# Performance work log

Measured on AMD Instinct MI355X. Metric: run time of the kernel, lower is better.

The kernel has to match this reference:

```python
import jax, jax.numpy as jnp
import numpy as np

V, H, B, T = 64, 128, 128, 512


def setup_inputs() -> dict:
    key = jax.random.key(0)
    ks = jax.random.split(key, 12)
    s = 0.05
    return {
        "x": jax.random.randint(ks[0], (B, T), 0, V),
        "emb": jax.random.normal(ks[1], (V, H), dtype=jnp.float32) * s,
        "w_ih_f": jax.random.normal(ks[2], (4 * H, H), dtype=jnp.float32) * s,
        "w_hh_f": jax.random.normal(ks[3], (4 * H, H), dtype=jnp.float32) * s,
        "b_ih_f": jax.random.normal(ks[4], (4 * H,), dtype=jnp.float32) * s,
        "b_hh_f": jax.random.normal(ks[5], (4 * H,), dtype=jnp.float32) * s,
        "w_ih_b": jax.random.normal(ks[6], (4 * H, H), dtype=jnp.float32) * s,
        "w_hh_b": jax.random.normal(ks[7], (4 * H, H), dtype=jnp.float32) * s,
        "b_ih_b": jax.random.normal(ks[8], (4 * H,), dtype=jnp.float32) * s,
        "b_hh_b": jax.random.normal(ks[9], (4 * H,), dtype=jnp.float32) * s,
        "fc_w": jax.random.normal(ks[10], (V, 2 * H), dtype=jnp.float32) * s,
        "fc_b": jax.random.normal(ks[11], (V,), dtype=jnp.float32) * s,
    }


def _lstm_scan(xp, w_hh):
    # xp: [T, B, 4H] precomputed input projections (+ biases); w_hh: [4H, H]
    h_dim = w_hh.shape[1]
    b = xp.shape[1]
    h0 = jnp.zeros((b, h_dim), dtype=xp.dtype)
    c0 = jnp.zeros((b, h_dim), dtype=xp.dtype)

    def step(carry, xt):
        h, c = carry
        gates = xt + h @ w_hh.T  # [B, 4H]
        i, f, g, o = jnp.split(gates, 4, axis=-1)  # torch gate order: i, f, g, o
        i = jax.nn.sigmoid(i)
        f = jax.nn.sigmoid(f)
        g = jnp.tanh(g)
        o = jax.nn.sigmoid(o)
        c = f * c + i * g
        h = o * jnp.tanh(c)
        return (h, c), h

    _, hs = jax.lax.scan(step, (h0, c0), xp)
    return hs  # [T, B, H]


def reference(x, emb, w_ih_f, w_hh_f, b_ih_f, b_hh_f,
              w_ih_b, w_hh_b, b_ih_b, b_hh_b, fc_w, fc_b):
    # embedding lookup: [B, T, H]
    e = emb[x]
    # precompute gate input projections for both directions
    xp_f = jnp.einsum('bth,gh->tbg', e, w_ih_f) + (b_ih_f + b_hh_f)  # [T,B,4H]
    xp_b = jnp.einsum('bth,gh->tbg', e, w_ih_b) + (b_ih_b + b_hh_b)
    h_f = _lstm_scan(xp_f, w_hh_f)                    # [T, B, H]
    h_b = _lstm_scan(xp_b[::-1], w_hh_b)[::-1]        # reversed-time dir, flipped back
    out = jnp.concatenate([h_f, h_b], axis=-1)        # [T, B, 2H]
    out = jnp.transpose(out, (1, 0, 2))               # [B, T, 2H]
    return out @ fc_w.T + fc_b                        # [B, T, V]
```

## Files before the change

kernel.cpp:

```cpp
#include <hip/hip_runtime.h>
#include <hip/hip_bf16.h>

#define B_ 128
#define T_ 512
#define H_ 128
#define V_ 64
#define G4_ 512

typedef _Float16 h2_t __attribute__((ext_vector_type(2)));
typedef _Float16 h8_t __attribute__((ext_vector_type(8)));
struct h8s { h2_t p[4]; };

__device__ __forceinline__ float dot2f(h2_t a, h2_t b, float c) {
#if __has_builtin(__builtin_amdgcn_fdot2)
  return __builtin_amdgcn_fdot2(a, b, c, false);
#else
  return fmaf((float)a[1], (float)b[1], fmaf((float)a[0], (float)b[0], c));
#endif
}

__device__ __forceinline__ float ex2(float x) {
#if __has_builtin(__builtin_amdgcn_exp2f)
  return __builtin_amdgcn_exp2f(x);
#else
  return exp2f(x);
#endif
}

__device__ __forceinline__ float rcpf_(float x) {
#if __has_builtin(__builtin_amdgcn_rcpf)
  return __builtin_amdgcn_rcpf(x);
#else
  return 1.0f / x;
#endif
}

#define QP_XOR1 0xB1
#define QP_XOR2 0x4E
#define QP_BC0 0x00
#define QP_BC1 0x55
#define QP_BC2 0xAA
#define QP_BC3 0xFF

template <int CTRL>
__device__ __forceinline__ float qperm(float v) {
#if __has_builtin(__builtin_amdgcn_update_dpp)
  return __builtin_bit_cast(
      float, __builtin_amdgcn_update_dpp(0, __builtin_bit_cast(int, v), CTRL,
                                         0xf, 0xf, true));
#else
  int lane = (int)(threadIdx.x & 3);
  int src;
  if constexpr (CTRL == QP_XOR1) src = lane ^ 1;
  else if constexpr (CTRL == QP_XOR2) src = lane ^ 2;
  else src = CTRL & 3;
  return __shfl(v, ((int)threadIdx.x & ~3) + src, 64);
#endif
}

__global__ __launch_bounds__(512) void k_tables(
    const float* __restrict__ emb,
    const float* __restrict__ w_ih_f, const float* __restrict__ b_ih_f,
    const float* __restrict__ b_hh_f,
    const float* __restrict__ w_ih_b, const float* __restrict__ b_ih_b,
    const float* __restrict__ b_hh_b,
    float* __restrict__ Ptab) {
  const int dir = blockIdx.x >> 6;
  const int v = blockIdx.x & 63;
  const int j = threadIdx.x;
  const float* w_ih = dir ? w_ih_b : w_ih_f;
  const float* bi = dir ? b_ih_b : b_ih_f;
  const float* bh = dir ? b_hh_b : b_hh_f;
  const float4* e4 = (const float4*)(emb + v * H_);
  const float4* w4 = (const float4*)(w_ih + j * H_);
  float a0 = 0.f, a1 = 0.f, a2 = 0.f, a3 = 0.f;
#pragma unroll
  for (int q = 0; q < H_ / 4; ++q) {
    float4 e = e4[q];
    float4 w = w4[q];
    a0 = fmaf(e.x, w.x, a0);
    a1 = fmaf(e.y, w.y, a1);
    a2 = fmaf(e.z, w.z, a2);
    a3 = fmaf(e.w, w.w, a3);
  }
  const int g = j >> 7, k = j & 127;
  Ptab[dir * (V_ * G4_) + v * G4_ + (k << 2) + g] =
      (a0 + a1) + (a2 + a3) + bi[j] + bh[j];
}

__global__ __launch_bounds__(512, 1) void k_scan(
    const int* __restrict__ x,
    const float* __restrict__ w_hh_f,
    const float* __restrict__ w_hh_b,
    const float* __restrict__ Ptab,
    _Float16* __restrict__ hs) {
  __shared__ __align__(16) float P[V_ * G4_];
  __shared__ int xoff[T_];
  __shared__ __align__(16) _Float16 hb[2][H_];
  __shared__ __align__(16) _Float16 hist[64][H_];

  const int tid = threadIdx.x;
  const int b = blockIdx.x >> 1;
  const int dir = blockIdx.x & 1;
  const int l = tid & 63;
  const int w = tid >> 6;
  const int g = l & 3;
  const int k = (w << 4) + (l >> 2);
  const int k4g = (k << 2) + g;

  {
    const float4* src = (const float4*)(Ptab + dir * (V_ * G4_));
    float4* dst = (float4*)P;
#pragma unroll
    for (int i = 0; i < (V_ * G4_ / 4) / 512; ++i)
      dst[tid + i * 512] = src[tid + i * 512];
  }
  xoff[tid] = x[(b << 9) + tid] << 9;
  if (tid < H_) hb[0][tid] = (_Float16)0.f;

  const float* W = dir ? w_hh_b : w_hh_f;
  h2_t wr[4][16];
#pragma unroll
  for (int j = 0; j < 4; ++j) {
    const float2* wp = (const float2*)(W + (j * H_ + k) * H_ + g * 32);
#pragma unroll
    for (int e = 0; e < 16; ++e) {
      float2 ww = wp[e];
      wr[j][e] = h2_t{(_Float16)ww.x, (_Float16)ww.y};
    }
  }

  const float nm = (g == 2) ? -2.8853900817779268f : -1.4426950408889634f;
  const float sa = (g == 2) ? 2.f : 1.f;
  const float sb = (g == 2) ? -1.f : 0.f;

  float c0 = 0.f;

  __syncthreads();

  float pv = P[xoff[dir ? (T_ - 1) : 0] + k4g];

  int cur = 0;
  for (int s = 0; s < T_; ++s) {
    const int t = dir ? (T_ - 1 - s) : s;
    const h8_t* hq8 = (const h8_t*)(&hb[cur][g << 5]);
    h8s q0 = __builtin_bit_cast(h8s, hq8[0]);
    h8s q1 = __builtin_bit_cast(h8s, hq8[1]);
    h8s q2 = __builtin_bit_cast(h8s, hq8[2]);
    h8s q3 = __builtin_bit_cast(h8s, hq8[3]);

    const int sn = (s < T_ - 1) ? s + 1 : s;
    const int tn = dir ? (T_ - 1 - sn) : sn;
    const float pvn = P[xoff[tn] + k4g];

    float a0 = 0.f, a1 = 0.f, a2 = 0.f, a3 = 0.f;
#pragma unroll
    for (int e = 0; e < 4; ++e) {
      a0 = dot2f(q0.p[e], wr[0][e], a0);
      a1 = dot2f(q0.p[e], wr[1][e], a1);
      a2 = dot2f(q0.p[e], wr[2][e], a2);
      a3 = dot2f(q0.p[e], wr[3][e], a3);
    }
#pragma unroll
    for (int e = 0; e < 4; ++e) {
      a0 = dot2f(q1.p[e], wr[0][4 + e], a0);
      a1 = dot2f(q1.p[e], wr[1][4 + e], a1);
      a2 = dot2f(q1.p[e], wr[2][4 + e], a2);
      a3 = dot2f(q1.p[e], wr[3][4 + e], a3);
    }
#pragma unroll
    for (int e = 0; e < 4; ++e) {
      a0 = dot2f(q2.p[e], wr[0][8 + e], a0);
      a1 = dot2f(q2.p[e], wr[1][8 + e], a1);
      a2 = dot2f(q2.p[e], wr[2][8 + e], a2);
      a3 = dot2f(q2.p[e], wr[3][8 + e], a3);
    }
#pragma unroll
    for (int e = 0; e < 4; ++e) {
      a0 = dot2f(q3.p[e], wr[0][12 + e], a0);
      a1 = dot2f(q3.p[e], wr[1][12 + e], a1);
      a2 = dot2f(q3.p[e], wr[2][12 + e], a2);
      a3 = dot2f(q3.p[e], wr[3][12 + e], a3);
    }

    float s0 = a0 + qperm<QP_XOR1>(a0);
    float s1 = a1 + qperm<QP_XOR1>(a1);
    float s2 = a2 + qperm<QP_XOR1>(a2);
    float s3 = a3 + qperm<QP_XOR1>(a3);
    float A = (g & 1) ? s1 : s0;
    float Bv = (g & 1) ? s3 : s2;
    float A2 = A + qperm<QP_XOR2>(A);
    float B2 = Bv + qperm<QP_XOR2>(Bv);
    float gv = ((g & 2) ? B2 : A2) + pv;

    float e0 = ex2(nm * gv);
    float r0 = rcpf_(1.f + e0);
    float y = fmaf(sa, r0, sb);

    float yi = qperm<QP_BC0>(y);
    float yf = qperm<QP_BC1>(y);
    float yg = qperm<QP_BC2>(y);
    float yo = qperm<QP_BC3>(y);

    c0 = fmaf(yf, c0, yi * yg);
    float ec = ex2(-2.8853900817779268f * c0);
    float rc = rcpf_(1.f + ec);
    float tc = fmaf(2.f, rc, -1.f);
    float ht = yo * tc;

    if (g == 0) {
      _Float16 hh = (_Float16)ht;
      hb[cur ^ 1][k] = hh;
      hist[t & 63][k] = hh;
    }

    if ((s & 63) == 63) {
      __syncthreads();
      const int base = t & ~63;
#pragma unroll
      for (int it = 0; it < 2; ++it) {
        int idx = it * 512 + tid;
        int tl = idx >> 4, q = idx & 15;
        h8_t v8 = *(const h8_t*)(&hist[tl][q << 3]);
        *(h8_t*)(hs + (((size_t)((b << 9) + base + tl)) << 8) + (dir << 7) +
                 (q << 3)) = v8;
      }
    }
    __syncthreads();
    pv = pvn;
    cur ^= 1;
  }
}

__global__ __launch_bounds__(256) void k_fc(
    const _Float16* __restrict__ hs,
    const float* __restrict__ fc_w,
    const float* __restrict__ fc_b,
    float* __restrict__ out) {
  __shared__ __align__(16) _Float16 Wl[V_ * 2 * H_];
  __shared__ float bl[V_];
  const int tid = threadIdx.x;
  for (int i = tid; i < V_ * 2 * H_; i += 256) Wl[i] = (_Float16)fc_w[i];
  if (tid < V_) bl[tid] = fc_b[tid];
  __syncthreads();

  const size_t row = (size_t)blockIdx.x * 256 + tid;
  const h8_t* h8 = (const h8_t*)(hs + (row << 8));
  float acc[V_];
#pragma unroll
  for (int v = 0; v < V_; ++v) acc[v] = 0.f;

  for (int ch = 0; ch < 8; ++ch) {
    h8s hv0 = __builtin_bit_cast(h8s, h8[ch * 4 + 0]);
    h8s hv1 = __builtin_bit_cast(h8s, h8[ch * 4 + 1]);
    h8s hv2 = __builtin_bit_cast(h8s, h8[ch * 4 + 2]);
    h8s hv3 = __builtin_bit_cast(h8s, h8[ch * 4 + 3]);
#pragma unroll
    for (int v = 0; v < V_; ++v) {
      const h8_t* w8 = (const h8_t*)(Wl + v * 256 + ch * 32);
      float a = acc[v];
      h8s wv = __builtin_bit_cast(h8s, w8[0]);
      a = dot2f(hv0.p[0], wv.p[0], a);
      a = dot2f(hv0.p[1], wv.p[1], a);
      a = dot2f(hv0.p[2], wv.p[2], a);
      a = dot2f(hv0.p[3], wv.p[3], a);
      wv = __builtin_bit_cast(h8s, w8[1]);
      a = dot2f(hv1.p[0], wv.p[0], a);
      a = dot2f(hv1.p[1], wv.p[1], a);
      a = dot2f(hv1.p[2], wv.p[2], a);
      a = dot2f(hv1.p[3], wv.p[3], a);
      wv = __builtin_bit_cast(h8s, w8[2]);
      a = dot2f(hv2.p[0], wv.p[0], a);
      a = dot2f(hv2.p[1], wv.p[1], a);
      a = dot2f(hv2.p[2], wv.p[2], a);
      a = dot2f(hv2.p[3], wv.p[3], a);
      wv = __builtin_bit_cast(h8s, w8[3]);
      a = dot2f(hv3.p[0], wv.p[0], a);
      a = dot2f(hv3.p[1], wv.p[1], a);
      a = dot2f(hv3.p[2], wv.p[2], a);
      a = dot2f(hv3.p[3], wv.p[3], a);
      acc[v] = a;
    }
  }
  float* orow = out + (row << 6);
#pragma unroll
  for (int v = 0; v < V_; v += 4) {
    float4 o = make_float4(acc[v] + bl[v], acc[v + 1] + bl[v + 1],
                           acc[v + 2] + bl[v + 2], acc[v + 3] + bl[v + 3]);
    *(float4*)(orow + v) = o;
  }
}

extern "C" void kernel_launch(void* const* d_in, const int* in_sizes, int n_in,
                              void* d_out, int out_size, void* d_ws, size_t ws_size,
                              hipStream_t stream) {
  const int* x = (const int*)d_in[0];
  const float* emb = (const float*)d_in[1];
  const float* w_ih_f = (const float*)d_in[2];
  const float* w_hh_f = (const float*)d_in[3];
  const float* b_ih_f = (const float*)d_in[4];
  const float* b_hh_f = (const float*)d_in[5];
  const float* w_ih_b = (const float*)d_in[6];
  const float* w_hh_b = (const float*)d_in[7];
  const float* b_ih_b = (const float*)d_in[8];
  const float* b_hh_b = (const float*)d_in[9];
  const float* fc_w = (const float*)d_in[10];
  const float* fc_b = (const float*)d_in[11];
  float* out = (float*)d_out;

  float* Ptab = (float*)d_ws;
  _Float16* hs = (_Float16*)((char*)d_ws + (size_t)2 * V_ * G4_ * sizeof(float));

  k_tables<<<2 * V_, G4_, 0, stream>>>(emb, w_ih_f, b_ih_f, b_hh_f, w_ih_b,
                                       b_ih_b, b_hh_b, Ptab);
  k_scan<<<B_ * 2, G4_, 0, stream>>>(x, w_hh_f, w_hh_b, Ptab, hs);
  k_fc<<<B_ * T_ / 256, 256, 0, stream>>>(hs, fc_w, fc_b, out);
}
```

Before: 352.4 us.

## Pack two batch sequences per 1024-thread scan block sharing LDS table

The scan kernel now runs two batch rows of the same direction in one 1024-thread block, sharing a single copy of the projection table in LDS. Per-half buffers for hidden state, history and token offsets are added, and the history flush interval drops to 32 steps. This halves the grid and the table staging traffic, and gives more waves per CU to hide the recurrent step latency. The risks are that half the CUs sit idle, each CU carries twice the ALU work, and barriers now cover 1024 threads.

```diff
diff --git a/kernel.cpp b/kernel.cpp
--- a/kernel.cpp
+++ b/kernel.cpp
@@ -88,22 +88,24 @@
       (a0 + a1) + (a2 + a3) + bi[j] + bh[j];
 }
 
-__global__ __launch_bounds__(512, 1) void k_scan(
+__global__ __launch_bounds__(1024, 1) void k_scan(
     const int* __restrict__ x,
     const float* __restrict__ w_hh_f,
     const float* __restrict__ w_hh_b,
     const float* __restrict__ Ptab,
     _Float16* __restrict__ hs) {
   __shared__ __align__(16) float P[V_ * G4_];
-  __shared__ int xoff[T_];
-  __shared__ __align__(16) _Float16 hb[2][H_];
-  __shared__ __align__(16) _Float16 hist[64][H_];
+  __shared__ int xoff[2][T_];
+  __shared__ __align__(16) _Float16 hb[2][2][H_];
+  __shared__ __align__(16) _Float16 hist[2][32][H_];
 
   const int tid = threadIdx.x;
-  const int b = blockIdx.x >> 1;
-  const int dir = blockIdx.x & 1;
-  const int l = tid & 63;
-  const int w = tid >> 6;
+  const int half = tid >> 9;
+  const int lt = tid & 511;
+  const int dir = blockIdx.x >> 6;
+  const int b = ((blockIdx.x & 63) << 1) + half;
+  const int l = lt & 63;
+  const int w = lt >> 6;
   const int g = l & 3;
   const int k = (w << 4) + (l >> 2);
   const int k4g = (k << 2) + g;
@@ -112,11 +114,11 @@
     const float4* src = (const float4*)(Ptab + dir * (V_ * G4_));
     float4* dst = (float4*)P;
 #pragma unroll
-    for (int i = 0; i < (V_ * G4_ / 4) / 512; ++i)
-      dst[tid + i * 512] = src[tid + i * 512];
-  }
-  xoff[tid] = x[(b << 9) + tid] << 9;
-  if (tid < H_) hb[0][tid] = (_Float16)0.f;
+    for (int i = 0; i < (V_ * G4_ / 4) / 1024; ++i)
+      dst[tid + i * 1024] = src[tid + i * 1024];
+  }
+  xoff[half][lt] = x[(b << 9) + lt] << 9;
+  if (lt < H_) hb[half][0][lt] = (_Float16)0.f;
 
   const float* W = dir ? w_hh_b : w_hh_f;
   h2_t wr[4][16];
@@ -138,12 +140,12 @@
 
   __syncthreads();
 
-  float pv = P[xoff[dir ? (T_ - 1) : 0] + k4g];
+  float pv = P[xoff[half][dir ? (T_ - 1) : 0] + k4g];
 
   int cur = 0;
   for (int s = 0; s < T_; ++s) {
     const int t = dir ? (T_ - 1 - s) : s;
-    const h8_t* hq8 = (const h8_t*)(&hb[cur][g << 5]);
+    const h8_t* hq8 = (const h8_t*)(&hb[half][cur][g << 5]);
     h8s q0 = __builtin_bit_cast(h8s, hq8[0]);
     h8s q1 = __builtin_bit_cast(h8s, hq8[1]);
     h8s q2 = __builtin_bit_cast(h8s, hq8[2]);
@@ -151,7 +153,7 @@
 
     const int sn = (s < T_ - 1) ? s + 1 : s;
     const int tn = dir ? (T_ - 1 - sn) : sn;
-    const float pvn = P[xoff[tn] + k4g];
+    const float pvn = P[xoff[half][tn] + k4g];
 
     float a0 = 0.f, a1 = 0.f, a2 = 0.f, a3 = 0.f;
 #pragma unroll
@@ -210,21 +212,17 @@
 
     if (g == 0) {
       _Float16 hh = (_Float16)ht;
-      hb[cur ^ 1][k] = hh;
-      hist[t & 63][k] = hh;
-    }
-
-    if ((s & 63) == 63) {
+      hb[half][cur ^ 1][k] = hh;
+      hist[half][t & 31][k] = hh;
+    }
+
+    if ((s & 31) == 31) {
       __syncthreads();
-      const int base = t & ~63;
-#pragma unroll
-      for (int it = 0; it < 2; ++it) {
-        int idx = it * 512 + tid;
-        int tl = idx >> 4, q = idx & 15;
-        h8_t v8 = *(const h8_t*)(&hist[tl][q << 3]);
-        *(h8_t*)(hs + (((size_t)((b << 9) + base + tl)) << 8) + (dir << 7) +
-                 (q << 3)) = v8;
-      }
+      const int base = t & ~31;
+      const int tl = lt >> 4, q = lt & 15;
+      h8_t v8 = *(const h8_t*)(&hist[half][tl][q << 3]);
+      *(h8_t*)(hs + (((size_t)((b << 9) + base + tl)) << 8) + (dir << 7) +
+               (q << 3)) = v8;
     }
     __syncthreads();
     pv = pvn;
@@ -313,6 +311,6 @@
 
   k_tables<<<2 * V_, G4_, 0, stream>>>(emb, w_ih_f, b_ih_f, b_hh_f, w_ih_b,
                                        b_ih_b, b_hh_b, Ptab);
-  k_scan<<<B_ * 2, G4_, 0, stream>>>(x, w_hh_f, w_hh_b, Ptab, hs);
+  k_scan<<<B_, 1024, 0, stream>>>(x, w_hh_f, w_hh_b, Ptab, hs);
   k_fc<<<B_ * T_ / 256, 256, 0, stream>>>(hs, fc_w, fc_b, out);
 }
```

Result: slower. 538.4 us (+52.8%).
